# Optimization experiments

Measured on AMD Instinct MI355X. Metric: run time of the kernel, lower is better.

## Reference

```python
import jax, jax.numpy as jnp
import numpy as np

NEG_SLOPE = 0.01  # torch LeakyReLU default
LN_EPS = 1e-5
L2_EPS = 1e-12  # torch F.normalize eps


def setup_inputs() -> dict:
    key = jax.random.key(0)
    ks = jax.random.split(key, 8)
    B, T, N, C = 16, 32, 64, 256
    local_feat = jax.random.normal(ks[0], (B, T, N, C), dtype=jnp.float32)
    global_feat = jax.random.normal(ks[1], (B, C), dtype=jnp.float32)
    pos = jax.random.normal(ks[2], (B, T * N, 3), dtype=jnp.float32)
    adj_w = jax.random.normal(ks[3], (C, C), dtype=jnp.float32) * (1.0 / np.sqrt(C))
    affine_w = jax.random.normal(ks[4], (C, C), dtype=jnp.float32) * np.sqrt(2.0 / C)  # kaiming-ish
    affine_b = jnp.zeros((C,), dtype=jnp.float32)
    ln_g = jnp.ones((C,), dtype=jnp.float32)
    ln_b = jnp.zeros((C,), dtype=jnp.float32)
    return {"local_feat": local_feat, "global_feat": global_feat, "pos": pos,
            "adj_w": adj_w, "affine_w": affine_w, "affine_b": affine_b,
            "ln_g": ln_g, "ln_b": ln_b}


def reference(local_feat, global_feat, pos, adj_w, affine_w, affine_b, ln_g, ln_b):
    B, T, N, C = local_feat.shape
    x = local_feat.reshape(B, T * N, C)  # [B, M, C]
    # L2 normalize along features
    nrm = jnp.sqrt(jnp.sum(x * x, axis=-1, keepdims=True))
    nf = x / jnp.maximum(nrm, L2_EPS)
    # bilinear scores: A = nf @ W @ nf^T  -> [B, M, M]
    A = jnp.einsum('bnc,cd,bmd->bnm', nf, adj_w, nf)
    A = 5.0 * (A - jnp.max(A, axis=-1, keepdims=True))
    A = jax.nn.softmax(A, axis=-1)
    # affine projection (torch Linear: x @ W^T + b)
    h = jnp.einsum('bmc,dc->bmd', x, affine_w) + affine_b
    # aggregation
    h = jnp.einsum('bnm,bmc->bnc', A, h)
    # LayerNorm + LeakyReLU
    mu = jnp.mean(h, axis=-1, keepdims=True)
    var = jnp.mean(jnp.square(h - mu), axis=-1, keepdims=True)
    h = (h - mu) / jnp.sqrt(var + LN_EPS) * ln_g + ln_b
    h = jnp.where(h >= 0, h, NEG_SLOPE * h)
    return h.reshape(B, T, N, C)
```

## Files before the change

### kernel.cpp

```cpp
#include <hip/hip_runtime.h>
#include <hip/hip_bf16.h>
#include <stdint.h>

#define B_  16
#define M_  2048
#define C_  256
#define BM_ 32768

typedef __bf16 bf16x8 __attribute__((ext_vector_type(8)));
typedef __bf16 bf16x2 __attribute__((ext_vector_type(2)));
typedef float  f32x4  __attribute__((ext_vector_type(4)));
typedef float  f32x16 __attribute__((ext_vector_type(16)));
typedef unsigned int uint2v __attribute__((ext_vector_type(2)));

__device__ __forceinline__ unsigned short f2bf(float f) {
    uint32_t u = __builtin_bit_cast(uint32_t, f);
    u += 0x7fffu + ((u >> 16) & 1u);
    return (unsigned short)(u >> 16);
}

__device__ __forceinline__ uint32_t pkbf(float a, float b) {
    bf16x2 t; t[0] = (__bf16)a; t[1] = (__bf16)b;
    return __builtin_bit_cast(uint32_t, t);
}

__device__ __forceinline__ float bf2f(unsigned short u) {
    return __builtin_bit_cast(float, ((uint32_t)u) << 16);
}

__device__ __forceinline__ void gload16(const void* g, void* l) {
    __builtin_amdgcn_global_load_lds(
        (const __attribute__((address_space(1))) void*)g,
        (__attribute__((address_space(3))) void*)l, 16, 0, 0);
}

__device__ __forceinline__ void publish_barrier() {
    asm volatile("s_waitcnt vmcnt(0)" ::: "memory");
    __builtin_amdgcn_sched_barrier(0);
    __syncthreads();
    __builtin_amdgcn_sched_barrier(0);
}

__global__ void prep_weights(const float* __restrict__ adj,
                             const float* __restrict__ affw,
                             unsigned short* __restrict__ adjT5,
                             unsigned short* __restrict__ affwB) {
    int idx = blockIdx.x * 256 + threadIdx.x;
    int d = idx >> 8, c = idx & 255;
    adjT5[d * 256 + c] = f2bf(7.2134752f * adj[c * 256 + d]);
    affwB[idx] = f2bf(affw[idx]);
}

__global__ void l2norm_kernel(const float* __restrict__ x,
                              unsigned short* __restrict__ nf,
                              float* __restrict__ norms) {
    int w = threadIdx.x >> 6, lane = threadIdx.x & 63;
    int row = blockIdx.x * 4 + w;
    const float4 v = *reinterpret_cast<const float4*>(x + (size_t)row * 256 + lane * 4);
    float ss = v.x * v.x + v.y * v.y + v.z * v.z + v.w * v.w;
    #pragma unroll
    for (int m = 1; m < 64; m <<= 1) ss += __shfl_xor(ss, m);
    float nrm = sqrtf(ss);
    float s = 1.0f / fmaxf(nrm, 1e-12f);
    ushort4 o;
    o.x = f2bf(v.x * s); o.y = f2bf(v.y * s); o.z = f2bf(v.z * s); o.w = f2bf(v.w * s);
    *reinterpret_cast<ushort4*>(nf + (size_t)row * 256 + lane * 4) = o;
    if (lane == 0) norms[row] = nrm;
}

__global__ __launch_bounds__(512, 2)
void dual_gemm(const unsigned short* __restrict__ A,
               const unsigned short* __restrict__ B1,
               const unsigned short* __restrict__ B2,
               const float* __restrict__ norms,
               const float* __restrict__ bias,
               unsigned short* __restrict__ outQ,
               unsigned short* __restrict__ outV3,
               unsigned short* __restrict__ outK3) {
    __shared__ unsigned short bb1[256 * 56];
    __shared__ unsigned short bb2[256 * 56];
    int tid = threadIdx.x;
    int w = tid >> 6, lane = tid & 63, g = lane >> 4, r = lane & 15;
    int m0 = blockIdx.x * 128;

    const f32x4 z = {0.f, 0.f, 0.f, 0.f};
    f32x4 accq[16], accv[16];
    #pragma unroll
    for (int i = 0; i < 16; i++) { accq[i] = z; accv[i] = z; }

    int row = m0 + w * 16 + r;
    int kvblk_r = row >> 5, mrow = row & 31;

    for (int dc = 0; dc < 8; dc++) {
        __syncthreads();
        #pragma unroll
        for (int it = 0; it < 2; it++) {
            int n = (w * 2 + it) * 16 + (lane >> 2);
            int t = lane & 3;
            *reinterpret_cast<uint4*>(&bb1[n * 56 + t * 8]) =
                *reinterpret_cast<const uint4*>(B1 + (size_t)n * 256 + dc * 32 + t * 8);
            *reinterpret_cast<uint4*>(&bb2[n * 56 + t * 8]) =
                *reinterpret_cast<const uint4*>(B2 + (size_t)n * 256 + dc * 32 + t * 8);
        }
        __syncthreads();
        bf16x8 af = *reinterpret_cast<const bf16x8*>(
            A + (size_t)row * 256 + dc * 32 + g * 8);
        {
            int ch = dc * 2 + (g >> 1);
            int khl = g & 1;
            *reinterpret_cast<bf16x8*>(
                outK3 + (size_t)kvblk_r * 8192 + ch * 512 + (khl * 32 + mrow) * 8) = af;
        }
        #pragma unroll
        for (int nf16 = 0; nf16 < 16; nf16++) {
            bf16x8 b1f = *reinterpret_cast<const bf16x8*>(&bb1[(nf16 * 16 + r) * 56 + g * 8]);
            accq[nf16] = __builtin_amdgcn_mfma_f32_16x16x32_bf16(af, b1f, accq[nf16], 0, 0, 0);
            bf16x8 b2f = *reinterpret_cast<const bf16x8*>(&bb2[(nf16 * 16 + r) * 56 + g * 8]);
            accv[nf16] = __builtin_amdgcn_mfma_f32_16x16x32_bf16(af, b2f, accv[nf16], 0, 0, 0);
        }
    }
    #pragma unroll
    for (int nf16 = 0; nf16 < 16; nf16++) {
        int n = nf16 * 16 + r;
        #pragma unroll
        for (int j = 0; j < 4; j++) {
            int m = m0 + w * 16 + g * 4 + j;
            outQ[(size_t)m * 256 + n] = f2bf(accq[nf16][j]);
        }
    }
    int mm = m0 + w * 16 + g * 4;
    int kvblk = mm >> 5;
    int kv0 = mm & 31;
    int jj  = kv0 >> 4;
    int hl2 = (kv0 >> 3) & 1;
    int e0  = kv0 & 7;
    float4 nr = *reinterpret_cast<const float4*>(norms + mm);
    #pragma unroll
    for (int nf16 = 0; nf16 < 16; nf16++) {
        int n = nf16 * 16 + r;
        int cb = n >> 5, mr2 = n & 31;
        int slot = (cb * 2 + jj) * 64 + hl2 * 32 + mr2;
        float bv = bias[n];
        ushort4 o;
        o.x = f2bf(accv[nf16][0] * nr.x + bv);
        o.y = f2bf(accv[nf16][1] * nr.y + bv);
        o.z = f2bf(accv[nf16][2] * nr.z + bv);
        o.w = f2bf(accv[nf16][3] * nr.w + bv);
        *reinterpret_cast<ushort4*>(outV3 + (size_t)kvblk * 8192 + slot * 8 + e0) = o;
    }
}

__global__ __launch_bounds__(256, 2)
void flash_kernel(const unsigned short* __restrict__ Q,
                  const unsigned short* __restrict__ K3,
                  const unsigned short* __restrict__ V3,
                  float* __restrict__ out,
                  unsigned short* __restrict__ part1,
                  float* __restrict__ ml) {
    __shared__ __align__(16) char smem[65536];
    const int tid = threadIdx.x;
    const int w = tid >> 6, lane = tid & 63;
    const int hl = lane >> 5, m = lane & 31;
    const int blk = blockIdx.x;
    const int idx = blk >> 3;
    const int b = (blk & 7) * 2 + (idx >> 5);
    const int sub = idx & 31;
    const int mblk = sub >> 1, h = sub & 1;
    const int q0 = b * M_ + mblk * 128 + w * 32;

    bf16x8 qf[16];
    #pragma unroll
    for (int ch = 0; ch < 16; ch++)
        qf[ch] = *reinterpret_cast<const bf16x8*>(
            Q + (size_t)(q0 + m) * 256 + ch * 16 + hl * 8);

    const f32x16 z16 = {0,0,0,0, 0,0,0,0, 0,0,0,0, 0,0,0,0};
    f32x16 acc[8];
    #pragma unroll
    for (int cb = 0; cb < 8; cb++) acc[cb] = z16;
    float lsum = 0.0f;

    const unsigned short* Ksrc =
        K3 + ((size_t)(b * 64 + h * 32) * 1024 + tid) * 8;
    const unsigned short* Vsrc =
        V3 + ((size_t)(b * 64 + h * 32) * 1024 + tid) * 8;

    auto stageK = [&](int step, int buf) {
        char* kb = smem + buf * 16384;
        const unsigned short* src = Ksrc + (size_t)step * 8192;
        #pragma unroll
        for (int it = 0; it < 4; it++)
            gload16(src + it * 2048, kb + (it * 256 + w * 64) * 16);
    };
    auto stageV = [&](int step, int buf) {
        char* vb = smem + 32768 + buf * 16384;
        const unsigned short* src = Vsrc + (size_t)step * 8192;
        #pragma unroll
        for (int it = 0; it < 4; it++)
            gload16(src + it * 2048, vb + (it * 256 + w * 64) * 16);
    };

    stageK(0, 0); stageV(0, 0);
    publish_barrier();
    stageK(1, 1); stageV(1, 1);

    for (int step = 0; step < 32; step++) {
        const int cur = step & 1;
        const char* kbl = smem + cur * 16384 + lane * 16;
        const char* vbl = smem + 32768 + cur * 16384 + lane * 16;

        f32x16 sf = z16;
        __builtin_amdgcn_s_setprio(1);
        #pragma unroll
        for (int ch = 0; ch < 16; ch++) {
            bf16x8 kf = *reinterpret_cast<const bf16x8*>(kbl + ch * 1024);
            sf = __builtin_amdgcn_mfma_f32_32x32x16_bf16(kf, qf[ch], sf, 0, 0, 0);
        }
        __builtin_amdgcn_s_setprio(0);

        #pragma unroll
        for (int i = 0; i < 16; i++) {
            sf[i] = exp2f(sf[i]);
            lsum += sf[i];
        }
        uint32_t pk0 = pkbf(sf[0], sf[1]),   pk1 = pkbf(sf[2], sf[3]);
        uint32_t pk2 = pkbf(sf[4], sf[5]),   pk3 = pkbf(sf[6], sf[7]);
        uint32_t pk4 = pkbf(sf[8], sf[9]),   pk5 = pkbf(sf[10], sf[11]);
        uint32_t pk6 = pkbf(sf[12], sf[13]), pk7 = pkbf(sf[14], sf[15]);
        uint2v r0 = __builtin_amdgcn_permlane32_swap(pk0, pk2, false, false);
        uint2v r1 = __builtin_amdgcn_permlane32_swap(pk1, pk3, false, false);
        uint2v r2 = __builtin_amdgcn_permlane32_swap(pk4, pk6, false, false);
        uint2v r3 = __builtin_amdgcn_permlane32_swap(pk5, pk7, false, false);
        uint4 u0; u0.x = r0[0]; u0.y = r1[0]; u0.z = r0[1]; u0.w = r1[1];
        uint4 u1; u1.x = r2[0]; u1.y = r3[0]; u1.z = r2[1]; u1.w = r3[1];
        bf16x8 pf0 = __builtin_bit_cast(bf16x8, u0);
        bf16x8 pf1 = __builtin_bit_cast(bf16x8, u1);

        __builtin_amdgcn_s_setprio(1);
        #pragma unroll
        for (int cb = 0; cb < 8; cb++) {
            bf16x8 v0 = *reinterpret_cast<const bf16x8*>(vbl + (cb * 2 + 0) * 1024);
            acc[cb] = __builtin_amdgcn_mfma_f32_32x32x16_bf16(v0, pf0, acc[cb], 0, 0, 0);
            bf16x8 v1 = *reinterpret_cast<const bf16x8*>(vbl + (cb * 2 + 1) * 1024);
            acc[cb] = __builtin_amdgcn_mfma_f32_32x32x16_bf16(v1, pf1, acc[cb], 0, 0, 0);
        }
        __builtin_amdgcn_s_setprio(0);

        publish_barrier();
        if (step + 2 < 32) {
            stageK(step + 2, cur);
            stageV(step + 2, cur);
        }
    }

    lsum += __shfl_xor(lsum, 32);
    float inv = 1.0f / lsum;
    float wgt = lsum;
    size_t qrow = (size_t)(q0 + m);
    if (h == 0) {
        #pragma unroll
        for (int cb = 0; cb < 8; cb++)
            #pragma unroll
            for (int q4 = 0; q4 < 4; q4++) {
                int c0i = cb * 32 + q4 * 8 + 4 * hl;
                float4 o;
                o.x = acc[cb][q4 * 4 + 0] * inv;
                o.y = acc[cb][q4 * 4 + 1] * inv;
                o.z = acc[cb][q4 * 4 + 2] * inv;
                o.w = acc[cb][q4 * 4 + 3] * inv;
                *reinterpret_cast<float4*>(out + qrow * 256 + c0i) = o;
            }
        if (hl == 0) ml[qrow] = wgt;
    } else {
        #pragma unroll
        for (int cb = 0; cb < 8; cb++)
            #pragma unroll
            for (int q4 = 0; q4 < 4; q4++) {
                int c0i = cb * 32 + q4 * 8 + 4 * hl;
                uint2 u;
                u.x = pkbf(acc[cb][q4 * 4 + 0] * inv, acc[cb][q4 * 4 + 1] * inv);
                u.y = pkbf(acc[cb][q4 * 4 + 2] * inv, acc[cb][q4 * 4 + 3] * inv);
                *reinterpret_cast<uint2*>(part1 + qrow * 256 + c0i) = u;
            }
        if (hl == 0) ml[BM_ + qrow] = wgt;
    }
}

__global__ void merge_ln_kernel(const unsigned short* __restrict__ part1,
                                const float* __restrict__ ml,
                                const float* __restrict__ gam,
                                const float* __restrict__ bet,
                                float* __restrict__ out) {
    int w = threadIdx.x >> 6, lane = threadIdx.x & 63;
    size_t row = (size_t)blockIdx.x * 4 + w;
    float w0 = ml[row], w1 = ml[BM_ + row];
    float rs = 1.0f / (w0 + w1);
    float4 o0 = *reinterpret_cast<float4*>(out + row * 256 + lane * 4);
    ushort4 p = *reinterpret_cast<const ushort4*>(part1 + row * 256 + lane * 4);
    float4 v;
    v.x = (w0 * o0.x + w1 * bf2f(p.x)) * rs;
    v.y = (w0 * o0.y + w1 * bf2f(p.y)) * rs;
    v.z = (w0 * o0.z + w1 * bf2f(p.z)) * rs;
    v.w = (w0 * o0.w + w1 * bf2f(p.w)) * rs;
    float s = v.x + v.y + v.z + v.w;
    float q = v.x * v.x + v.y * v.y + v.z * v.z + v.w * v.w;
    #pragma unroll
    for (int m = 1; m < 64; m <<= 1) { s += __shfl_xor(s, m); q += __shfl_xor(q, m); }
    float mu = s * (1.0f / 256.0f);
    float var = q * (1.0f / 256.0f) - mu * mu;
    float rstd = rsqrtf(var + 1e-5f);
    float4 gg = *reinterpret_cast<const float4*>(gam + lane * 4);
    float4 bb = *reinterpret_cast<const float4*>(bet + lane * 4);
    float4 o;
    o.x = (v.x - mu) * rstd * gg.x + bb.x;
    o.y = (v.y - mu) * rstd * gg.y + bb.y;
    o.z = (v.z - mu) * rstd * gg.z + bb.z;
    o.w = (v.w - mu) * rstd * gg.w + bb.w;
    o.x = o.x >= 0.f ? o.x : 0.01f * o.x;
    o.y = o.y >= 0.f ? o.y : 0.01f * o.y;
    o.z = o.z >= 0.f ? o.z : 0.01f * o.z;
    o.w = o.w >= 0.f ? o.w : 0.01f * o.w;
    *reinterpret_cast<float4*>(out + row * 256 + lane * 4) = o;
}

extern "C" void kernel_launch(void* const* d_in, const int* in_sizes, int n_in,
                              void* d_out, int out_size, void* d_ws, size_t ws_size,
                              hipStream_t stream) {
    const float* local_feat = (const float*)d_in[0];
    const float* adj_w    = (const float*)d_in[3];
    const float* affine_w = (const float*)d_in[4];
    const float* affine_b = (const float*)d_in[5];
    const float* ln_g     = (const float*)d_in[6];
    const float* ln_b     = (const float*)d_in[7];
    float* out = (float*)d_out;

    char* ws = (char*)d_ws;
    unsigned short* nf    = (unsigned short*)(ws);
    unsigned short* q     = (unsigned short*)(ws + 16777216);
    unsigned short* v3    = (unsigned short*)(ws + 33554432);
    float*          norms = (float*)         (ws + 50331648);
    unsigned short* adjT5 = (unsigned short*)(ws + 50462720);
    unsigned short* affw  = (unsigned short*)(ws + 50593792);
    unsigned short* k3    = (unsigned short*)(ws + 50724864);
    unsigned short* part1 = (unsigned short*)(ws);
    float*          ml    = (float*)         (ws + 50462720);

    prep_weights<<<256, 256, 0, stream>>>(adj_w, affine_w, adjT5, affw);
    l2norm_kernel<<<BM_ / 4, 256, 0, stream>>>(local_feat, nf, norms);
    dual_gemm<<<BM_ / 128, 512, 0, stream>>>(nf, adjT5, affw, norms, affine_b, q, v3, k3);
    flash_kernel<<<512, 256, 0, stream>>>(q, k3, v3, out, part1, ml);
    merge_ln_kernel<<<BM_ / 4, 256, 0, stream>>>(part1, ml, ln_g, ln_b, out);
}
```

Before: 131.9 us.

## Fuse split-KV merge and LayerNorm into flash kernel via last-block atomic flag

```diff
diff --git a/kernel.cpp b/kernel.cpp
--- a/kernel.cpp
+++ b/kernel.cpp
@@ -155,9 +155,15 @@
                   const unsigned short* __restrict__ K3,
                   const unsigned short* __restrict__ V3,
                   float* __restrict__ out,
+                  unsigned short* __restrict__ part0,
                   unsigned short* __restrict__ part1,
-                  float* __restrict__ ml) {
+                  float* __restrict__ ml,
+                  int* __restrict__ flags,
+                  const float* __restrict__ gam,
+                  const float* __restrict__ bet,
+                  int fused) {
     __shared__ __align__(16) char smem[65536];
+    __shared__ int lastFlag;
     const int tid = threadIdx.x;
     const int w = tid >> 6, lane = tid & 63;
     const int hl = lane >> 5, m = lane & 31;
@@ -257,21 +263,9 @@
     float inv = 1.0f / lsum;
     float wgt = lsum;
     size_t qrow = (size_t)(q0 + m);
-    if (h == 0) {
-        #pragma unroll
-        for (int cb = 0; cb < 8; cb++)
-            #pragma unroll
-            for (int q4 = 0; q4 < 4; q4++) {
-                int c0i = cb * 32 + q4 * 8 + 4 * hl;
-                float4 o;
-                o.x = acc[cb][q4 * 4 + 0] * inv;
-                o.y = acc[cb][q4 * 4 + 1] * inv;
-                o.z = acc[cb][q4 * 4 + 2] * inv;
-                o.w = acc[cb][q4 * 4 + 3] * inv;
-                *reinterpret_cast<float4*>(out + qrow * 256 + c0i) = o;
-            }
-        if (hl == 0) ml[qrow] = wgt;
-    } else {
+
+    if (fused) {
+        unsigned short* myp = h ? part1 : part0;
         #pragma unroll
         for (int cb = 0; cb < 8; cb++)
             #pragma unroll
@@ -280,9 +274,109 @@
                 uint2 u;
                 u.x = pkbf(acc[cb][q4 * 4 + 0] * inv, acc[cb][q4 * 4 + 1] * inv);
                 u.y = pkbf(acc[cb][q4 * 4 + 2] * inv, acc[cb][q4 * 4 + 3] * inv);
-                *reinterpret_cast<uint2*>(part1 + qrow * 256 + c0i) = u;
+                *reinterpret_cast<uint2*>(myp + qrow * 256 + c0i) = u;
             }
-        if (hl == 0) ml[BM_ + qrow] = wgt;
+        if (hl == 0) ml[h * BM_ + qrow] = wgt;
+        __threadfence();
+        if (tid == 0)
+            lastFlag = (atomicAdd(&flags[b * 16 + mblk], 1) == 1);
+        __syncthreads();
+        if (lastFlag) {
+            __threadfence();
+            float w0 = ml[qrow], w1 = ml[BM_ + qrow];
+            float rs = 1.0f / (w0 + w1);
+            float a0 = w0 * rs, a1 = w1 * rs;
+            const unsigned short* p0 = part0 + qrow * 256 + hl * 128;
+            const unsigned short* p1 = part1 + qrow * 256 + hl * 128;
+            float s = 0.0f, ssq = 0.0f;
+            #pragma unroll 4
+            for (int k = 0; k < 16; k++) {
+                uint4 u0 = *reinterpret_cast<const uint4*>(p0 + k * 8);
+                uint4 u1 = *reinterpret_cast<const uint4*>(p1 + k * 8);
+                const uint32_t* a = &u0.x;
+                const uint32_t* c = &u1.x;
+                #pragma unroll
+                for (int j = 0; j < 4; j++) {
+                    float v0 = a0 * bf2f((unsigned short)(a[j] & 0xffff))
+                             + a1 * bf2f((unsigned short)(c[j] & 0xffff));
+                    float v1 = a0 * bf2f((unsigned short)(a[j] >> 16))
+                             + a1 * bf2f((unsigned short)(c[j] >> 16));
+                    s += v0 + v1; ssq += v0 * v0 + v1 * v1;
+                }
+            }
+            s   += __shfl_xor(s, 32);
+            ssq += __shfl_xor(ssq, 32);
+            float mu = s * (1.0f / 256.0f);
+            float var = ssq * (1.0f / 256.0f) - mu * mu;
+            float rstd = rsqrtf(var + 1e-5f);
+            #pragma unroll 4
+            for (int k = 0; k < 16; k++) {
+                uint4 u0 = *reinterpret_cast<const uint4*>(p0 + k * 8);
+                uint4 u1 = *reinterpret_cast<const uint4*>(p1 + k * 8);
+                const uint32_t* a = &u0.x;
+                const uint32_t* c = &u1.x;
+                int c0i = hl * 128 + k * 8;
+                float4 g0 = *reinterpret_cast<const float4*>(gam + c0i);
+                float4 g1 = *reinterpret_cast<const float4*>(gam + c0i + 4);
+                float4 b0 = *reinterpret_cast<const float4*>(bet + c0i);
+                float4 b1 = *reinterpret_cast<const float4*>(bet + c0i + 4);
+                float vv[8];
+                #pragma unroll
+                for (int j = 0; j < 4; j++) {
+                    vv[2 * j]     = a0 * bf2f((unsigned short)(a[j] & 0xffff))
+                                  + a1 * bf2f((unsigned short)(c[j] & 0xffff));
+                    vv[2 * j + 1] = a0 * bf2f((unsigned short)(a[j] >> 16))
+                                  + a1 * bf2f((unsigned short)(c[j] >> 16));
+                }
+                float4 o0, o1;
+                o0.x = (vv[0] - mu) * rstd * g0.x + b0.x;
+                o0.y = (vv[1] - mu) * rstd * g0.y + b0.y;
+                o0.z = (vv[2] - mu) * rstd * g0.z + b0.z;
+                o0.w = (vv[3] - mu) * rstd * g0.w + b0.w;
+                o1.x = (vv[4] - mu) * rstd * g1.x + b1.x;
+                o1.y = (vv[5] - mu) * rstd * g1.y + b1.y;
+                o1.z = (vv[6] - mu) * rstd * g1.z + b1.z;
+                o1.w = (vv[7] - mu) * rstd * g1.w + b1.w;
+                o0.x = o0.x >= 0.f ? o0.x : 0.01f * o0.x;
+                o0.y = o0.y >= 0.f ? o0.y : 0.01f * o0.y;
+                o0.z = o0.z >= 0.f ? o0.z : 0.01f * o0.z;
+                o0.w = o0.w >= 0.f ? o0.w : 0.01f * o0.w;
+                o1.x = o1.x >= 0.f ? o1.x : 0.01f * o1.x;
+                o1.y = o1.y >= 0.f ? o1.y : 0.01f * o1.y;
+                o1.z = o1.z >= 0.f ? o1.z : 0.01f * o1.z;
+                o1.w = o1.w >= 0.f ? o1.w : 0.01f * o1.w;
+                *reinterpret_cast<float4*>(out + qrow * 256 + c0i) = o0;
+                *reinterpret_cast<float4*>(out + qrow * 256 + c0i + 4) = o1;
+            }
+        }
+    } else {
+        if (h == 0) {
+            #pragma unroll
+            for (int cb = 0; cb < 8; cb++)
+                #pragma unroll
+                for (int q4 = 0; q4 < 4; q4++) {
+                    int c0i = cb * 32 + q4 * 8 + 4 * hl;
+                    float4 o;
+                    o.x = acc[cb][q4 * 4 + 0] * inv;
+                    o.y = acc[cb][q4 * 4 + 1] * inv;
+                    o.z = acc[cb][q4 * 4 + 2] * inv;
+                    o.w = acc[cb][q4 * 4 + 3] * inv;
+                    *reinterpret_cast<float4*>(out + qrow * 256 + c0i) = o;
+                }
+            if (hl == 0) ml[qrow] = wgt;
+        } else {
+            #pragma unroll
+            for (int cb = 0; cb < 8; cb++)
+                #pragma unroll
+                for (int q4 = 0; q4 < 4; q4++) {
+                    int c0i = cb * 32 + q4 * 8 + 4 * hl;
+                    uint2 u;
+                    u.x = pkbf(acc[cb][q4 * 4 + 0] * inv, acc[cb][q4 * 4 + 1] * inv);
+                    u.y = pkbf(acc[cb][q4 * 4 + 2] * inv, acc[cb][q4 * 4 + 3] * inv);
+                    *reinterpret_cast<uint2*>(part1 + qrow * 256 + c0i) = u;
+                }
+            if (hl == 0) ml[BM_ + qrow] = wgt;
+        }
     }
 }
 
@@ -342,12 +436,21 @@
     unsigned short* adjT5 = (unsigned short*)(ws + 50462720);
     unsigned short* affw  = (unsigned short*)(ws + 50593792);
     unsigned short* k3    = (unsigned short*)(ws + 50724864);
-    unsigned short* part1 = (unsigned short*)(ws);
+    unsigned short* part0 = (unsigned short*)(ws);
     float*          ml    = (float*)         (ws + 50462720);
+
+    const size_t need = 67502080ull + 16777216ull + 4096ull;
+    int fused = (ws_size >= need) ? 1 : 0;
+    unsigned short* part1 = fused ? (unsigned short*)(ws + 67502080)
+                                  : (unsigned short*)(ws);
+    int* flags = (int*)(ws + 67502080 + 16777216);
 
     prep_weights<<<256, 256, 0, stream>>>(adj_w, affine_w, adjT5, affw);
     l2norm_kernel<<<BM_ / 4, 256, 0, stream>>>(local_feat, nf, norms);
     dual_gemm<<<BM_ / 128, 512, 0, stream>>>(nf, adjT5, affw, norms, affine_b, q, v3, k3);
-    flash_kernel<<<512, 256, 0, stream>>>(q, k3, v3, out, part1, ml);
-    merge_ln_kernel<<<BM_ / 4, 256, 0, stream>>>(part1, ml, ln_g, ln_b, out);
-}
+    if (fused) hipMemsetAsync(flags, 0, 256 * sizeof(int), stream);
+    flash_kernel<<<512, 256, 0, stream>>>(q, k3, v3, out, part0, part1, ml, flags,
+                                          ln_g, ln_b, fused);
+    if (!fused)
+        merge_ln_kernel<<<BM_ / 4, 256, 0, stream>>>(part1, ml, ln_g, ln_b, out);
+}
```

Measured after the change: 340.9 us. +158.5%, slower.

## Fuse L2 normalization into dual GEMM and store both flash halves as bf16

Applied to the files above, without the earlier changes.

```diff
diff --git a/kernel.cpp b/kernel.cpp
--- a/kernel.cpp
+++ b/kernel.cpp
@@ -51,45 +51,64 @@
     affwB[idx] = f2bf(affw[idx]);
 }
 
-__global__ void l2norm_kernel(const float* __restrict__ x,
-                              unsigned short* __restrict__ nf,
-                              float* __restrict__ norms) {
-    int w = threadIdx.x >> 6, lane = threadIdx.x & 63;
-    int row = blockIdx.x * 4 + w;
-    const float4 v = *reinterpret_cast<const float4*>(x + (size_t)row * 256 + lane * 4);
-    float ss = v.x * v.x + v.y * v.y + v.z * v.z + v.w * v.w;
-    #pragma unroll
-    for (int m = 1; m < 64; m <<= 1) ss += __shfl_xor(ss, m);
-    float nrm = sqrtf(ss);
-    float s = 1.0f / fmaxf(nrm, 1e-12f);
-    ushort4 o;
-    o.x = f2bf(v.x * s); o.y = f2bf(v.y * s); o.z = f2bf(v.z * s); o.w = f2bf(v.w * s);
-    *reinterpret_cast<ushort4*>(nf + (size_t)row * 256 + lane * 4) = o;
-    if (lane == 0) norms[row] = nrm;
-}
-
-__global__ __launch_bounds__(512, 2)
-void dual_gemm(const unsigned short* __restrict__ A,
-               const unsigned short* __restrict__ B1,
-               const unsigned short* __restrict__ B2,
-               const float* __restrict__ norms,
-               const float* __restrict__ bias,
-               unsigned short* __restrict__ outQ,
-               unsigned short* __restrict__ outV3,
-               unsigned short* __restrict__ outK3) {
+__global__ __launch_bounds__(512, 1)
+void fused_gemm(const float* __restrict__ X,
+                const unsigned short* __restrict__ B1,
+                const unsigned short* __restrict__ B2,
+                const float* __restrict__ bias,
+                unsigned short* __restrict__ outQ,
+                unsigned short* __restrict__ outV3,
+                unsigned short* __restrict__ outK3) {
     __shared__ unsigned short bb1[256 * 56];
     __shared__ unsigned short bb2[256 * 56];
     int tid = threadIdx.x;
     int w = tid >> 6, lane = tid & 63, g = lane >> 4, r = lane & 15;
     int m0 = blockIdx.x * 128;
+    int row = m0 + w * 16 + r;
+    int kvblk_r = row >> 5, mrow = row & 31;
+
+    float4 xv[16];
+    float ss = 0.0f;
+    #pragma unroll
+    for (int dc = 0; dc < 8; dc++) {
+        xv[2 * dc]     = *reinterpret_cast<const float4*>(
+            X + (size_t)row * 256 + dc * 32 + g * 8);
+        xv[2 * dc + 1] = *reinterpret_cast<const float4*>(
+            X + (size_t)row * 256 + dc * 32 + g * 8 + 4);
+        ss += xv[2 * dc].x     * xv[2 * dc].x     + xv[2 * dc].y     * xv[2 * dc].y
+            + xv[2 * dc].z     * xv[2 * dc].z     + xv[2 * dc].w     * xv[2 * dc].w
+            + xv[2 * dc + 1].x * xv[2 * dc + 1].x + xv[2 * dc + 1].y * xv[2 * dc + 1].y
+            + xv[2 * dc + 1].z * xv[2 * dc + 1].z + xv[2 * dc + 1].w * xv[2 * dc + 1].w;
+    }
+    ss += __shfl_xor(ss, 16);
+    ss += __shfl_xor(ss, 32);
+    float nrm = sqrtf(ss);
+    float scale = 1.0f / fmaxf(nrm, 1e-12f);
+    float4 nr;
+    nr.x = __shfl(nrm, g * 4 + 0);
+    nr.y = __shfl(nrm, g * 4 + 1);
+    nr.z = __shfl(nrm, g * 4 + 2);
+    nr.w = __shfl(nrm, g * 4 + 3);
+
+    bf16x8 af[8];
+    #pragma unroll
+    for (int dc = 0; dc < 8; dc++) {
+        uint4 u;
+        u.x = pkbf(xv[2 * dc].x * scale,     xv[2 * dc].y * scale);
+        u.y = pkbf(xv[2 * dc].z * scale,     xv[2 * dc].w * scale);
+        u.z = pkbf(xv[2 * dc + 1].x * scale, xv[2 * dc + 1].y * scale);
+        u.w = pkbf(xv[2 * dc + 1].z * scale, xv[2 * dc + 1].w * scale);
+        af[dc] = __builtin_bit_cast(bf16x8, u);
+        int ch = dc * 2 + (g >> 1);
+        int khl = g & 1;
+        *reinterpret_cast<bf16x8*>(
+            outK3 + (size_t)kvblk_r * 8192 + ch * 512 + (khl * 32 + mrow) * 8) = af[dc];
+    }
 
     const f32x4 z = {0.f, 0.f, 0.f, 0.f};
     f32x4 accq[16], accv[16];
     #pragma unroll
     for (int i = 0; i < 16; i++) { accq[i] = z; accv[i] = z; }
-
-    int row = m0 + w * 16 + r;
-    int kvblk_r = row >> 5, mrow = row & 31;
 
     for (int dc = 0; dc < 8; dc++) {
         __syncthreads();
@@ -103,20 +122,12 @@
                 *reinterpret_cast<const uint4*>(B2 + (size_t)n * 256 + dc * 32 + t * 8);
         }
         __syncthreads();
-        bf16x8 af = *reinterpret_cast<const bf16x8*>(
-            A + (size_t)row * 256 + dc * 32 + g * 8);
-        {
-            int ch = dc * 2 + (g >> 1);
-            int khl = g & 1;
-            *reinterpret_cast<bf16x8*>(
-                outK3 + (size_t)kvblk_r * 8192 + ch * 512 + (khl * 32 + mrow) * 8) = af;
-        }
         #pragma unroll
         for (int nf16 = 0; nf16 < 16; nf16++) {
             bf16x8 b1f = *reinterpret_cast<const bf16x8*>(&bb1[(nf16 * 16 + r) * 56 + g * 8]);
-            accq[nf16] = __builtin_amdgcn_mfma_f32_16x16x32_bf16(af, b1f, accq[nf16], 0, 0, 0);
+            accq[nf16] = __builtin_amdgcn_mfma_f32_16x16x32_bf16(af[dc], b1f, accq[nf16], 0, 0, 0);
             bf16x8 b2f = *reinterpret_cast<const bf16x8*>(&bb2[(nf16 * 16 + r) * 56 + g * 8]);
-            accv[nf16] = __builtin_amdgcn_mfma_f32_16x16x32_bf16(af, b2f, accv[nf16], 0, 0, 0);
+            accv[nf16] = __builtin_amdgcn_mfma_f32_16x16x32_bf16(af[dc], b2f, accv[nf16], 0, 0, 0);
         }
     }
     #pragma unroll
@@ -134,7 +145,6 @@
     int jj  = kv0 >> 4;
     int hl2 = (kv0 >> 3) & 1;
     int e0  = kv0 & 7;
-    float4 nr = *reinterpret_cast<const float4*>(norms + mm);
     #pragma unroll
     for (int nf16 = 0; nf16 < 16; nf16++) {
         int n = nf16 * 16 + r;
@@ -155,8 +165,10 @@
                   const unsigned short* __restrict__ K3,
                   const unsigned short* __restrict__ V3,
                   float* __restrict__ out,
+                  unsigned short* __restrict__ part0,
                   unsigned short* __restrict__ part1,
-                  float* __restrict__ ml) {
+                  float* __restrict__ ml,
+                  int h0bf16) {
     __shared__ __align__(16) char smem[65536];
     const int tid = threadIdx.x;
     const int w = tid >> 6, lane = tid & 63;
@@ -255,9 +267,20 @@
 
     lsum += __shfl_xor(lsum, 32);
     float inv = 1.0f / lsum;
-    float wgt = lsum;
     size_t qrow = (size_t)(q0 + m);
-    if (h == 0) {
+    if (h0bf16 || h == 1) {
+        unsigned short* myp = h ? part1 : part0;
+        #pragma unroll
+        for (int cb = 0; cb < 8; cb++)
+            #pragma unroll
+            for (int q4 = 0; q4 < 4; q4++) {
+                int c0i = cb * 32 + q4 * 8 + 4 * hl;
+                uint2 u;
+                u.x = pkbf(acc[cb][q4 * 4 + 0] * inv, acc[cb][q4 * 4 + 1] * inv);
+                u.y = pkbf(acc[cb][q4 * 4 + 2] * inv, acc[cb][q4 * 4 + 3] * inv);
+                *reinterpret_cast<uint2*>(myp + qrow * 256 + c0i) = u;
+            }
+    } else {
         #pragma unroll
         for (int cb = 0; cb < 8; cb++)
             #pragma unroll
@@ -270,38 +293,40 @@
                 o.w = acc[cb][q4 * 4 + 3] * inv;
                 *reinterpret_cast<float4*>(out + qrow * 256 + c0i) = o;
             }
-        if (hl == 0) ml[qrow] = wgt;
-    } else {
-        #pragma unroll
-        for (int cb = 0; cb < 8; cb++)
-            #pragma unroll
-            for (int q4 = 0; q4 < 4; q4++) {
-                int c0i = cb * 32 + q4 * 8 + 4 * hl;
-                uint2 u;
-                u.x = pkbf(acc[cb][q4 * 4 + 0] * inv, acc[cb][q4 * 4 + 1] * inv);
-                u.y = pkbf(acc[cb][q4 * 4 + 2] * inv, acc[cb][q4 * 4 + 3] * inv);
-                *reinterpret_cast<uint2*>(part1 + qrow * 256 + c0i) = u;
-            }
-        if (hl == 0) ml[BM_ + qrow] = wgt;
-    }
-}
-
-__global__ void merge_ln_kernel(const unsigned short* __restrict__ part1,
+    }
+    if (hl == 0) ml[h * BM_ + qrow] = lsum;
+}
+
+__global__ void merge_ln_kernel(const unsigned short* __restrict__ part0,
+                                const unsigned short* __restrict__ part1,
                                 const float* __restrict__ ml,
                                 const float* __restrict__ gam,
                                 const float* __restrict__ bet,
-                                float* __restrict__ out) {
+                                float* __restrict__ out,
+                                int h0bf16) {
     int w = threadIdx.x >> 6, lane = threadIdx.x & 63;
-    size_t row = (size_t)blockIdx.x * 4 + w;
+    int blk = blockIdx.x;
+    int xcd = blk & 7, j = blk >> 3;
+    int b = 2 * xcd + (j >> 9);
+    size_t row = (size_t)b * 2048 + (size_t)(j & 511) * 4 + w;
     float w0 = ml[row], w1 = ml[BM_ + row];
     float rs = 1.0f / (w0 + w1);
-    float4 o0 = *reinterpret_cast<float4*>(out + row * 256 + lane * 4);
-    ushort4 p = *reinterpret_cast<const ushort4*>(part1 + row * 256 + lane * 4);
+    float a0 = w0 * rs, a1 = w1 * rs;
     float4 v;
-    v.x = (w0 * o0.x + w1 * bf2f(p.x)) * rs;
-    v.y = (w0 * o0.y + w1 * bf2f(p.y)) * rs;
-    v.z = (w0 * o0.z + w1 * bf2f(p.z)) * rs;
-    v.w = (w0 * o0.w + w1 * bf2f(p.w)) * rs;
+    ushort4 p1 = *reinterpret_cast<const ushort4*>(part1 + row * 256 + lane * 4);
+    if (h0bf16) {
+        ushort4 p0 = *reinterpret_cast<const ushort4*>(part0 + row * 256 + lane * 4);
+        v.x = a0 * bf2f(p0.x) + a1 * bf2f(p1.x);
+        v.y = a0 * bf2f(p0.y) + a1 * bf2f(p1.y);
+        v.z = a0 * bf2f(p0.z) + a1 * bf2f(p1.z);
+        v.w = a0 * bf2f(p0.w) + a1 * bf2f(p1.w);
+    } else {
+        float4 o0 = *reinterpret_cast<float4*>(out + row * 256 + lane * 4);
+        v.x = a0 * o0.x + a1 * bf2f(p1.x);
+        v.y = a0 * o0.y + a1 * bf2f(p1.y);
+        v.z = a0 * o0.z + a1 * bf2f(p1.z);
+        v.w = a0 * o0.w + a1 * bf2f(p1.w);
+    }
     float s = v.x + v.y + v.z + v.w;
     float q = v.x * v.x + v.y * v.y + v.z * v.z + v.w * v.w;
     #pragma unroll
@@ -335,19 +360,34 @@
     float* out = (float*)d_out;
 
     char* ws = (char*)d_ws;
-    unsigned short* nf    = (unsigned short*)(ws);
-    unsigned short* q     = (unsigned short*)(ws + 16777216);
-    unsigned short* v3    = (unsigned short*)(ws + 33554432);
-    float*          norms = (float*)         (ws + 50331648);
-    unsigned short* adjT5 = (unsigned short*)(ws + 50462720);
-    unsigned short* affw  = (unsigned short*)(ws + 50593792);
-    unsigned short* k3    = (unsigned short*)(ws + 50724864);
-    unsigned short* part1 = (unsigned short*)(ws);
-    float*          ml    = (float*)         (ws + 50462720);
+    unsigned short* q     = (unsigned short*)(ws);
+    unsigned short* v3    = (unsigned short*)(ws + 16777216);
+    unsigned short* k3    = (unsigned short*)(ws + 33554432);
+    unsigned short* part1;
+    unsigned short* part0;
+    unsigned short* adjT5;
+    unsigned short* affw;
+    float*          ml;
+
+    const size_t need = 84148224ull;
+    int h0bf16 = (ws_size >= need) ? 1 : 0;
+    if (h0bf16) {
+        part0 = (unsigned short*)(ws + 50331648);
+        part1 = (unsigned short*)(ws + 67108864);
+        adjT5 = (unsigned short*)(ws + 83886080);
+        affw  = (unsigned short*)(ws + 84017152);
+        ml    = (float*)         (ws + 83886080);
+    } else {
+        part0 = (unsigned short*)(ws + 50331648);
+        part1 = (unsigned short*)(ws + 50331648);
+        adjT5 = (unsigned short*)(ws + 67371008);
+        affw  = (unsigned short*)(ws + 67502080);
+        ml    = (float*)         (ws + 67108864);
+    }
 
     prep_weights<<<256, 256, 0, stream>>>(adj_w, affine_w, adjT5, affw);
-    l2norm_kernel<<<BM_ / 4, 256, 0, stream>>>(local_feat, nf, norms);
-    dual_gemm<<<BM_ / 128, 512, 0, stream>>>(nf, adjT5, affw, norms, affine_b, q, v3, k3);
-    flash_kernel<<<512, 256, 0, stream>>>(q, k3, v3, out, part1, ml);
-    merge_ln_kernel<<<BM_ / 4, 256, 0, stream>>>(part1, ml, ln_g, ln_b, out);
-}
+    fused_gemm<<<BM_ / 128, 512, 0, stream>>>(local_feat, adjT5, affw, affine_b,
+                                              q, v3, k3);
+    flash_kernel<<<512, 256, 0, stream>>>(q, k3, v3, out, part0, part1, ml, h0bf16);
+    merge_ln_kernel<<<8192, 256, 0, stream>>>(part0, part1, ml, ln_g, ln_b, out, h0bf16);
+}
```

New measurement: 176.0 us. +33.5%, slower.
